# Performance work log

Hardware: AMD Instinct MI355X
Metric: run time of the kernel (lower is better)

## Reference

```python
import jax, jax.numpy as jnp
import numpy as np

# thresholds from options['dist_threshold'] (init-time constants)
THRESHOLDS = jnp.array([0.5, 1.0], dtype=jnp.float32)

B, N, D, K = 16, 16384, 64, 64  # batch, h*w pixels, embed dim, n templates
N_CLASSES = 21


def setup_inputs() -> dict:
    key = jax.random.key(0)
    k1, k2, k3 = jax.random.split(key, 3)
    frame_embeddings = jax.random.normal(k1, (B, N, D), dtype=jnp.float32)
    templates = jax.random.normal(k2, (K, N, D), dtype=jnp.float32)
    template_classes = jax.random.randint(k3, (K,), 0, N_CLASSES, dtype=jnp.int64)
    return {
        "frame_embeddings": frame_embeddings,
        "templates": templates,
        "template_classes": template_classes,
    }


def reference(frame_embeddings, templates, template_classes):
    # Squared euclidean distance per pixel to each template, vectorized over K
    # [B,K,N,D] broadcast intermediate the torch loop also never materializes).
    x2 = jnp.sum(frame_embeddings * frame_embeddings, axis=-1)      # [B, N]
    t2 = jnp.sum(templates * templates, axis=-1)                    # [K, N]
    xt = jnp.einsum('bnd,knd->bkn', frame_embeddings, templates)    # [B, K, N]
    dists = x2[:, None, :] + t2[None, :, :] - 2.0 * xt              # [B, K, N]

    min_dists = jnp.min(dists, axis=1)                              # [B, N]
    min_idx = jnp.argmin(dists, axis=1)                             # [B, N]

    # One boolean mask per threshold, stacked: [T, B, N]
    masks = min_dists[None, :, :] <= THRESHOLDS[:, None, None]
    pred_classes = template_classes[min_idx]                        # [B, N]
    return masks, min_dists, pred_classes
```

## Files before the change

### kernel.cpp

```cpp
#include <hip/hip_runtime.h>
#include <stdint.h>


#define BB 16
#define NN 16384
#define DD 64
#define KK 64

typedef float v2f __attribute__((ext_vector_type(2)));

__global__ __launch_bounds__(128, 2)
void openset_kernel(const float* __restrict__ x,
                    const float* __restrict__ tmpl,
                    const int*   __restrict__ tcls,
                    float*       __restrict__ out) {
    __shared__ float4 st[KK * 32];
    __shared__ float4 sx[BB * 32];

    const int lane = threadIdx.x & 63;
    const int wv   = threadIdx.x >> 6;
    const int p0   = (int)(((blockIdx.x & 7) << 11) | ((blockIdx.x >> 3) << 1));
    const int p    = p0 + wv;

    const int half = lane >> 5;
    const int i32  = lane & 31;

#pragma unroll
    for (int c = 0; c < 16; ++c) {
        const int k = (wv * 16 + c) * 2 + half;
        const float4* src =
            (const float4*)(tmpl + ((size_t)k << 20)) + (size_t)p0 * 16;
        st[k * 32 + (i32 ^ (k & 7))] = src[i32];
    }
#pragma unroll
    for (int c = 0; c < 4; ++c) {
        const int b = (wv * 4 + c) * 2 + half;
        const float4* src =
            (const float4*)(x + ((size_t)b << 20)) + (size_t)p0 * 16;
        sx[b * 32 + i32] = src[i32];
    }
    __syncthreads();

    float4 t4[16];
#pragma unroll
    for (int j = 0; j < 16; ++j)
        t4[j] = st[lane * 32 + ((wv * 16 + j) ^ (lane & 7))];

    v2f acc[BB];
#pragma unroll
    for (int b = 0; b < BB; ++b) acc[b] = (v2f){0.f, 0.f};

#pragma unroll
    for (int h = 0; h < 2; ++h) {
#pragma unroll
        for (int b = 0; b < BB; ++b) {
            v2f a0 = (v2f){0.f, 0.f};
            v2f a1 = (v2f){0.f, 0.f};
#pragma unroll
            for (int j = 0; j < 8; ++j) {
                float4 xv = sx[b * 32 + wv * 16 + h * 8 + j];
                float4 tv = t4[h * 8 + j];
                v2f d0 = (v2f){xv.x - tv.x, xv.y - tv.y};
                v2f d1 = (v2f){xv.z - tv.z, xv.w - tv.w};
                a0 += d0 * d0;
                a1 += d1 * d1;
            }
            acc[b] += a0 + a1;
        }
    }

    float bestd = 0.f;
    int   bestk = 0;
#pragma unroll
    for (int b = 0; b < BB; ++b) {
        const float dme = acc[b].x + acc[b].y;
        float m = dme;
#pragma unroll
        for (int i = 1; i < 64; i <<= 1)
            m = fminf(m, __shfl_xor(m, i));
        const unsigned long long tie = __ballot(dme == m);
        const int ks = __ffsll(tie) - 1;
        if (lane == b) { bestd = m; bestk = ks; }
    }

    if (lane < BB) {
        const size_t BN = (size_t)BB * NN;
        const size_t o  = (size_t)lane * NN + p;
        out[o]          = (bestd <= 0.5f) ? 1.0f : 0.0f;
        out[BN + o]     = (bestd <= 1.0f) ? 1.0f : 0.0f;
        out[2 * BN + o] = bestd;
        out[3 * BN + o] = (float)tcls[bestk];
    }
}

extern "C" void kernel_launch(void* const* d_in, const int* in_sizes, int n_in,
                              void* d_out, int out_size, void* d_ws, size_t ws_size,
                              hipStream_t stream) {
    const float* x    = (const float*)d_in[0];
    const float* tmpl = (const float*)d_in[1];
    const int*   tcls = (const int*)d_in[2];
    float* out = (float*)d_out;

    dim3 grid(NN / 2);
    dim3 block(128);
    openset_kernel<<<grid, block, 0, stream>>>(x, tmpl, tcls, out);
}
```

Before: 410.1 us.

## Split per-block work across 8 waves, each owning 4 batches for one pixel

Grows the block from 2 to 8 wavefronts. Each wave now computes distances for 4 batch rows of one pixel instead of all 16, reading template values from shared memory inside the loop rather than caching 16 float4 in registers. Staging loads are spread over more waves. The aim is lower register pressure and more waves resident to hide memory latency. In exchange it issues more LDS reads per FMA and repeats the shuffle reduction across more waves.

```diff
diff --git a/kernel.cpp b/kernel.cpp
--- a/kernel.cpp
+++ b/kernel.cpp
@@ -9,7 +9,7 @@
 
 typedef float v2f __attribute__((ext_vector_type(2)));
 
-__global__ __launch_bounds__(128, 2)
+__global__ __launch_bounds__(512, 6)
 void openset_kernel(const float* __restrict__ x,
                     const float* __restrict__ tmpl,
                     const int*   __restrict__ tcls,
@@ -19,73 +19,72 @@
 
     const int lane = threadIdx.x & 63;
     const int wv   = threadIdx.x >> 6;
+    const int pp   = wv & 1;
+    const int q    = wv >> 1;
     const int p0   = (int)(((blockIdx.x & 7) << 11) | ((blockIdx.x >> 3) << 1));
-    const int p    = p0 + wv;
 
     const int half = lane >> 5;
     const int i32  = lane & 31;
 
 #pragma unroll
-    for (int c = 0; c < 16; ++c) {
-        const int k = (wv * 16 + c) * 2 + half;
+    for (int c = 0; c < 4; ++c) {
+        const int k = (wv * 4 + c) * 2 + half;
         const float4* src =
             (const float4*)(tmpl + ((size_t)k << 20)) + (size_t)p0 * 16;
         st[k * 32 + (i32 ^ (k & 7))] = src[i32];
     }
-#pragma unroll
-    for (int c = 0; c < 4; ++c) {
-        const int b = (wv * 4 + c) * 2 + half;
+    {
+        const int b = wv * 2 + half;
         const float4* src =
             (const float4*)(x + ((size_t)b << 20)) + (size_t)p0 * 16;
         sx[b * 32 + i32] = src[i32];
     }
     __syncthreads();
 
-    float4 t4[16];
+    v2f acc[4];
 #pragma unroll
-    for (int j = 0; j < 16; ++j)
-        t4[j] = st[lane * 32 + ((wv * 16 + j) ^ (lane & 7))];
-
-    v2f acc[BB];
-#pragma unroll
-    for (int b = 0; b < BB; ++b) acc[b] = (v2f){0.f, 0.f};
+    for (int i = 0; i < 4; ++i) acc[i] = (v2f){0.f, 0.f};
 
 #pragma unroll
     for (int h = 0; h < 2; ++h) {
+        v2f a0[4], a1[4];
 #pragma unroll
-        for (int b = 0; b < BB; ++b) {
-            v2f a0 = (v2f){0.f, 0.f};
-            v2f a1 = (v2f){0.f, 0.f};
+        for (int i = 0; i < 4; ++i) { a0[i] = (v2f){0.f, 0.f}; a1[i] = (v2f){0.f, 0.f}; }
 #pragma unroll
-            for (int j = 0; j < 8; ++j) {
-                float4 xv = sx[b * 32 + wv * 16 + h * 8 + j];
-                float4 tv = t4[h * 8 + j];
+        for (int j = 0; j < 8; ++j) {
+            const int e = pp * 16 + h * 8 + j;
+            const float4 tv = st[lane * 32 + (e ^ (lane & 7))];
+#pragma unroll
+            for (int i = 0; i < 4; ++i) {
+                const float4 xv = sx[(q * 4 + i) * 32 + e];
                 v2f d0 = (v2f){xv.x - tv.x, xv.y - tv.y};
                 v2f d1 = (v2f){xv.z - tv.z, xv.w - tv.w};
-                a0 += d0 * d0;
-                a1 += d1 * d1;
+                a0[i] += d0 * d0;
+                a1[i] += d1 * d1;
             }
-            acc[b] += a0 + a1;
         }
+#pragma unroll
+        for (int i = 0; i < 4; ++i) acc[i] += a0[i] + a1[i];
     }
 
     float bestd = 0.f;
     int   bestk = 0;
 #pragma unroll
-    for (int b = 0; b < BB; ++b) {
-        const float dme = acc[b].x + acc[b].y;
+    for (int i = 0; i < 4; ++i) {
+        const float dme = acc[i].x + acc[i].y;
         float m = dme;
 #pragma unroll
-        for (int i = 1; i < 64; i <<= 1)
-            m = fminf(m, __shfl_xor(m, i));
+        for (int s = 1; s < 64; s <<= 1)
+            m = fminf(m, __shfl_xor(m, s));
         const unsigned long long tie = __ballot(dme == m);
         const int ks = __ffsll(tie) - 1;
-        if (lane == b) { bestd = m; bestk = ks; }
+        if (lane == i) { bestd = m; bestk = ks; }
     }
 
-    if (lane < BB) {
+    if (lane < 4) {
+        const int b = q * 4 + lane;
         const size_t BN = (size_t)BB * NN;
-        const size_t o  = (size_t)lane * NN + p;
+        const size_t o  = (size_t)b * NN + (p0 + pp);
         out[o]          = (bestd <= 0.5f) ? 1.0f : 0.0f;
         out[BN + o]     = (bestd <= 1.0f) ? 1.0f : 0.0f;
         out[2 * BN + o] = bestd;
@@ -102,6 +101,6 @@
     float* out = (float*)d_out;
 
     dim3 grid(NN / 2);
-    dim3 block(128);
+    dim3 block(512);
     openset_kernel<<<grid, block, 0, stream>>>(x, tmpl, tcls, out);
 }
```

Result: faster. 400.4 us (-2.4%).
